# Kernel tuning notes

Hardware: AMD Instinct MI355X
Metric: run time of the kernel (lower is better)

## Reference

```python
import jax, jax.numpy as jnp
import numpy as np

D_MODEL = 1024
D_INNER = 2 * D_MODEL          # expand=2
D_STATE = 16
D_CONV = 4
DT_RANK = D_MODEL // 16        # ceil(1024/16)
BATCH, SEQ = 4, 1024
LN_EPS = 1e-5
LRELU_SLOPE = 0.01


def setup_inputs() -> dict:
    key = jax.random.key(0)
    ks = jax.random.split(key, 12)
    s = 0.02
    return {
        "x": jax.random.normal(ks[0], (BATCH, SEQ, D_MODEL), jnp.float32),
        "W_in": jax.random.normal(ks[1], (D_MODEL, 2 * D_INNER), jnp.float32) * s,
        "conv_w": jax.random.normal(ks[2], (D_INNER, D_CONV), jnp.float32) * s,
        "conv_b": jnp.zeros((D_INNER,), jnp.float32),
        "W_x": jax.random.normal(ks[3], (D_INNER, DT_RANK + 2 * D_STATE), jnp.float32) * s,
        "W_dt": jax.random.normal(ks[4], (DT_RANK, D_INNER), jnp.float32) * s,
        "b_dt": jax.random.normal(ks[5], (D_INNER,), jnp.float32) * 0.1 - 4.0,
        "A_log": jnp.log(jnp.broadcast_to(jnp.arange(1, D_STATE + 1, dtype=jnp.float32), (D_INNER, D_STATE))),
        "D": jnp.ones((D_INNER,), jnp.float32),
        "W_out": jax.random.normal(ks[6], (D_INNER, D_MODEL), jnp.float32) * s,
        "gamma": jnp.ones((D_MODEL,), jnp.float32),
        "beta": jnp.zeros((D_MODEL,), jnp.float32),
    }


def _selective_scan(u, dt, A, B, C, Dp):
    # u, dt: (b, l, d); A: (d, n); B, C: (b, l, n); Dp: (d,)
    dA = jnp.exp(dt[..., None] * A)                       # (b, l, d, n)
    dBu = dt[..., None] * B[:, :, None, :] * u[..., None]  # (b, l, d, n)

    def step(h, inp):
        dA_t, dBu_t, C_t = inp                            # (b,d,n),(b,d,n),(b,n)
        h = dA_t * h + dBu_t
        y = jnp.einsum("bdn,bn->bd", h, C_t)
        return h, y

    h0 = jnp.zeros((u.shape[0], u.shape[2], A.shape[1]), u.dtype)
    xs = (dA.transpose(1, 0, 2, 3), dBu.transpose(1, 0, 2, 3), C.transpose(1, 0, 2))
    _, ys = jax.lax.scan(step, h0, xs)                    # ys: (l, b, d)
    return ys.transpose(1, 0, 2) + u * Dp                 # (b, l, d)


def _mamba(x, W_in, conv_w, conv_b, W_x, W_dt, b_dt, A_log, Dp, W_out):
    xz = x @ W_in                                          # (b, l, 2*di)
    xc, z = jnp.split(xz, 2, axis=-1)
    # causal depthwise conv over time
    xc_t = xc.transpose(0, 2, 1)                           # (b, di, l)
    kern = conv_w[:, None, :]                              # (di, 1, k)
    conv = jax.lax.conv_general_dilated(
        xc_t, kern, window_strides=(1,), padding=[(D_CONV - 1, 0)],
        dimension_numbers=("NCH", "OIH", "NCH"), feature_group_count=D_INNER)
    xc = jax.nn.silu(conv + conv_b[None, :, None]).transpose(0, 2, 1)  # (b, l, di)

    x_dbl = xc @ W_x                                       # (b, l, dt_rank + 2n)
    dt, Bm, Cm = jnp.split(x_dbl, [DT_RANK, DT_RANK + D_STATE], axis=-1)
    dt = jax.nn.softplus(dt @ W_dt + b_dt)                 # (b, l, di)
    A = -jnp.exp(A_log)                                    # (di, n)

    y = _selective_scan(xc, dt, A, Bm, Cm, Dp)             # (b, l, di)
    y = y * jax.nn.silu(z)
    return y @ W_out                                       # (b, l, d_model)


def reference(x, W_in, conv_w, conv_b, W_x, W_dt, b_dt, A_log, D, W_out, gamma, beta):
    h = x + _mamba(x, W_in, conv_w, conv_b, W_x, W_dt, b_dt, A_log, D, W_out)
    mu = jnp.mean(h, axis=-1, keepdims=True)
    var = jnp.mean(jnp.square(h - mu), axis=-1, keepdims=True)
    h = (h - mu) * jax.lax.rsqrt(var + LN_EPS) * gamma + beta
    return jnp.where(h >= 0, h, LRELU_SLOPE * h)
```

## Files before the change

kernel.cpp:

```cpp
#include <hip/hip_runtime.h>
#include <hip/hip_fp16.h>
#include <cstdint>
#include <cstddef>

typedef _Float16 f16x8 __attribute__((ext_vector_type(8)));
typedef _Float16 f16x4 __attribute__((ext_vector_type(4)));
typedef float    f32x4 __attribute__((ext_vector_type(4)));

#define TC  32
#define NCH 32

__device__ __forceinline__ float sigmoidf_(float x) { return 1.f / (1.f + __expf(-x)); }

__device__ __forceinline__ void gload_lds16(const _Float16* g, _Float16* l) {
  __builtin_amdgcn_global_load_lds(
      (const __attribute__((address_space(1))) void*)g,
      (__attribute__((address_space(3))) void*)l, 16, 0, 0);
}

__device__ __forceinline__ void t16_body(const float* __restrict__ src,
    _Float16* __restrict__ dst, int R, int C, int Cpad, int bx, int by,
    int tid, float tile[32][33]) {
  int c0 = bx * 32, r0 = by * 32, tx = tid & 31, ty = tid >> 5;
  #pragma unroll
  for (int i = 0; i < 4; ++i) {
    int r = r0 + ty + i * 8, c = c0 + tx;
    tile[ty + i * 8][tx] = (r < R && c < C) ? src[(size_t)r * C + c] : 0.f;
  }
  __syncthreads();
  #pragma unroll
  for (int i = 0; i < 4; ++i) {
    int cc = c0 + ty + i * 8, rr = r0 + tx;
    if (cc < Cpad && rr < R) dst[(size_t)cc * R + rr] = (_Float16)tile[tx][ty + i * 8];
  }
}

__global__ __launch_bounds__(256) void k_prep(
    const float* __restrict__ x, _Float16* __restrict__ x16,
    const float* __restrict__ W_in, _Float16* __restrict__ WinT,
    const float* __restrict__ W_x, _Float16* __restrict__ WxT,
    const float* __restrict__ W_dt, _Float16* __restrict__ WdtT,
    const float* __restrict__ W_out, _Float16* __restrict__ WoutT)
{
  __shared__ float tile[32][33];
  const int blk = blockIdx.x, tid = threadIdx.x;
  if (blk < 4096) {
    int i = blk * 256 + tid;
    float4 v = ((const float4*)x)[i];
    f16x4 o = {(_Float16)v.x, (_Float16)v.y, (_Float16)v.z, (_Float16)v.w};
    ((f16x4*)x16)[i] = o;
  } else if (blk < 8192) {
    int b = blk - 4096;
    t16_body(W_in, WinT, 1024, 4096, 4096, b & 127, b >> 7, tid, tile);
  } else if (blk < 8448) {
    int b = blk - 8192;
    t16_body(W_x, WxT, 2048, 96, 128, b & 3, b >> 2, tid, tile);
  } else if (blk < 8576) {
    int b = blk - 8448;
    t16_body(W_dt, WdtT, 64, 2048, 2048, b & 63, b >> 6, tid, tile);
  } else {
    int b = blk - 8576;
    t16_body(W_out, WoutT, 2048, 1024, 1024, b & 31, b >> 5, tid, tile);
  }
}

template <int EPI>
__global__ __launch_bounds__(256) void k_gemm_bt(
    const _Float16* __restrict__ A,
    const _Float16* __restrict__ BT,
    float* __restrict__ C,
    _Float16* __restrict__ C16,
    _Float16* __restrict__ AUX,
    int M, int N, int K)
{
  __shared__ __align__(16) _Float16 As[128 * 64];
  __shared__ __align__(16) _Float16 Bs[128 * 64];
  const int tid  = threadIdx.x;
  const int lane = tid & 63;
  const int wave = tid >> 6;
  const int wm = (wave >> 1) * 64;
  const int wn = (wave & 1) * 64;
  const int l15 = lane & 15;
  const int q   = lane >> 4;
  const int m0 = blockIdx.y * 128;
  const int n0 = blockIdx.x * 128;

  const int kpb = K / gridDim.z;
  const int k0  = blockIdx.z * kpb;

  const int rch = lane >> 3;
  const int g   = (lane & 7) ^ (rch & 7);
  const _Float16* gA = A  + (size_t)(m0 + wave * 32 + rch) * K + k0 + g * 8;
  const _Float16* gB = BT + (size_t)(n0 + wave * 32 + rch) * K + k0 + g * 8;
  _Float16* lA = As + wave * 32 * 64 + lane * 8;
  _Float16* lB = Bs + wave * 32 * 64 + lane * 8;

  const int sx = l15 & 7;

  f32x4 acc[4][4] = {};

  for (int k = 0; k < kpb; k += 64) {
    #pragma unroll
    for (int c = 0; c < 4; ++c) {
      gload_lds16(gA + (size_t)(c * 8) * K + k, lA + c * 512);
      gload_lds16(gB + (size_t)(c * 8) * K + k, lB + c * 512);
    }
    __syncthreads();
    #pragma unroll
    for (int k32 = 0; k32 < 2; ++k32) {
      f16x8 af[4], bf[4];
      #pragma unroll
      for (int i = 0; i < 4; ++i) {
        af[i] = *(const f16x8*)&As[(wm + i * 16 + l15) * 64 + ((k32 * 4 + q) ^ sx) * 8];
        bf[i] = *(const f16x8*)&Bs[(wn + i * 16 + l15) * 64 + ((k32 * 4 + q) ^ sx) * 8];
      }
      #pragma unroll
      for (int mi = 0; mi < 4; ++mi)
        #pragma unroll
        for (int ni = 0; ni < 4; ++ni)
          acc[mi][ni] = __builtin_amdgcn_mfma_f32_16x16x32_f16(af[mi], bf[ni], acc[mi][ni], 0, 0, 0);
    }
    __syncthreads();
  }

  #pragma unroll
  for (int mi = 0; mi < 4; ++mi) {
    #pragma unroll
    for (int ni = 0; ni < 4; ++ni) {
      int col = n0 + wn + ni * 16 + l15;
      #pragma unroll
      for (int r = 0; r < 4; ++r) {
        int row = m0 + wm + mi * 16 + q * 4 + r;
        float v = acc[mi][ni][r];
        if constexpr (EPI == 3) {
          if (col < 2048) {
            C16[(size_t)row * 2048 + col] = (_Float16)v;
          } else {
            AUX[(size_t)row * 2048 + (col - 2048)] = (_Float16)(v * sigmoidf_(v));
          }
        } else {
          C[(size_t)blockIdx.z * M * N + (size_t)row * N + col] = v;
        }
      }
    }
  }
}

__global__ __launch_bounds__(256) void k_g3(
    const float* __restrict__ Cpart,
    const _Float16* __restrict__ BT,
    const float* __restrict__ bias,
    _Float16* __restrict__ AUX)
{
  __shared__ __align__(16) _Float16 As2[128 * 72];
  __shared__ __align__(16) _Float16 Bs[128 * 64];
  const int tid  = threadIdx.x;
  const int lane = tid & 63;
  const int wave = tid >> 6;
  const int wm = (wave >> 1) * 64;
  const int wn = (wave & 1) * 64;
  const int l15 = lane & 15;
  const int q   = lane >> 4;
  const int m0 = blockIdx.y * 128;
  const int n0 = blockIdx.x * 128;
  const int PL = 4096 * 128;

  #pragma unroll
  for (int i = 0; i < 4; ++i) {
    int idx = i * 256 + tid;
    int r = idx >> 3, s = idx & 7;
    const float* p = Cpart + (size_t)(m0 + r) * 128 + s * 8;
    f16x8 o;
    #pragma unroll
    for (int j = 0; j < 8; ++j)
      o[j] = (_Float16)(p[j] + p[j + PL] + p[j + 2 * PL] + p[j + 3 * PL]);
    *(f16x8*)&As2[r * 72 + s * 8] = o;
  }
  const int rch = lane >> 3;
  const int g   = (lane & 7) ^ (rch & 7);
  const _Float16* gB = BT + (size_t)(n0 + wave * 32 + rch) * 64 + g * 8;
  _Float16* lB = Bs + wave * 32 * 64 + lane * 8;
  #pragma unroll
  for (int c = 0; c < 4; ++c)
    gload_lds16(gB + (size_t)(c * 8) * 64, lB + c * 512);
  __syncthreads();

  const int sx = l15 & 7;
  f32x4 acc[4][4] = {};
  #pragma unroll
  for (int k32 = 0; k32 < 2; ++k32) {
    f16x8 af[4], bf[4];
    #pragma unroll
    for (int i = 0; i < 4; ++i) {
      af[i] = *(const f16x8*)&As2[(wm + i * 16 + l15) * 72 + (k32 * 4 + q) * 8];
      bf[i] = *(const f16x8*)&Bs[(wn + i * 16 + l15) * 64 + ((k32 * 4 + q) ^ sx) * 8];
    }
    #pragma unroll
    for (int mi = 0; mi < 4; ++mi)
      #pragma unroll
      for (int ni = 0; ni < 4; ++ni)
        acc[mi][ni] = __builtin_amdgcn_mfma_f32_16x16x32_f16(af[mi], bf[ni], acc[mi][ni], 0, 0, 0);
  }

  #pragma unroll
  for (int mi = 0; mi < 4; ++mi) {
    #pragma unroll
    for (int ni = 0; ni < 4; ++ni) {
      int col = n0 + wn + ni * 16 + l15;
      #pragma unroll
      for (int r = 0; r < 4; ++r) {
        int row = m0 + wm + mi * 16 + q * 4 + r;
        float t = acc[mi][ni][r] + bias[col];
        float sp = (t > 20.f) ? t : log1pf(__expf(t));
        AUX[(size_t)row * 2048 + col] = (_Float16)sp;
      }
    }
  }
}

__global__ __launch_bounds__(256) void k_conv_silu(
    const _Float16* __restrict__ xc, const float* __restrict__ cw,
    const float* __restrict__ cb, _Float16* __restrict__ out)
{
  int idx = blockIdx.x * 256 + threadIdx.x;
  int d = idx & 2047;
  int row = idx >> 11;
  int t = row & 1023;
  const _Float16* p = xc + (size_t)row * 2048 + d;
  float acc = cb[d] + cw[d * 4 + 3] * (float)p[0];
  if (t >= 1) acc += cw[d * 4 + 2] * (float)p[-2048];
  if (t >= 2) acc += cw[d * 4 + 1] * (float)p[-4096];
  if (t >= 3) acc += cw[d * 4 + 0] * (float)p[-6144];
  out[idx] = (_Float16)(acc * sigmoidf_(acc));
}

__global__ __launch_bounds__(256) void k_scan_part(
    const _Float16* __restrict__ dt, const _Float16* __restrict__ u,
    const float* __restrict__ Cpart, const float* __restrict__ A_log,
    float* __restrict__ P, float* __restrict__ S)
{
  const int tid = threadIdx.x;
  const int d = blockIdx.x * 256 + tid;
  const int c = blockIdx.y;
  const int b = blockIdx.z;
  const int row0 = b * 1024 + c * TC;
  const int PL = 4096 * 128;
  __shared__ float Bs[TC * 16];
  for (int i = tid; i < TC * 16; i += 256) {
    int t = i >> 4, n = i & 15;
    const float* p = Cpart + (size_t)(row0 + t) * 128 + 64 + n;
    Bs[i] = p[0] + p[PL] + p[2 * PL] + p[3 * PL];
  }
  float a[16];
  #pragma unroll
  for (int n = 0; n < 16; ++n) a[n] = -__expf(A_log[d * 16 + n]);
  float h[16] = {};
  float sumdt = 0.f;
  __syncthreads();
  for (int t = 0; t < TC; ++t) {
    const int row = row0 + t;
    float dtv = (float)dt[(size_t)row * 2048 + d];
    float uv  = (float)u[(size_t)row * 2048 + d];
    float dtu = dtv * uv;
    sumdt += dtv;
    #pragma unroll
    for (int n = 0; n < 16; ++n)
      h[n] = h[n] * __expf(dtv * a[n]) + dtu * Bs[t * 16 + n];
  }
  const size_t base = (size_t)(b * NCH + c) * 16 * 2048 + d;
  #pragma unroll
  for (int n = 0; n < 16; ++n) {
    P[base + n * 2048] = __expf(sumdt * a[n]);
    S[base + n * 2048] = h[n];
  }
}

__global__ __launch_bounds__(256) void k_scan_comb(
    float* __restrict__ P, const float* __restrict__ S)
{
  int idx = blockIdx.x * 256 + threadIdx.x;
  int d = idx & 2047;
  int n = (idx >> 11) & 15;
  int b = idx >> 15;
  float H = 0.f;
  for (int c = 0; c < NCH - 1; ++c) {
    size_t off = ((size_t)(b * NCH + c) * 16 + n) * 2048 + d;
    H = P[off] * H + S[off];
    P[off] = H;
  }
}

__global__ __launch_bounds__(256) void k_scan_y(
    const _Float16* dt, const _Float16* __restrict__ u,
    const _Float16* __restrict__ zs, const float* __restrict__ Cpart,
    const float* __restrict__ A_log, const float* __restrict__ Hbuf,
    const float* __restrict__ Dv, _Float16* ys)
{
  const int tid = threadIdx.x;
  const int d = blockIdx.x * 256 + tid;
  const int c = blockIdx.y;
  const int b = blockIdx.z;
  const int row0 = b * 1024 + c * TC;
  const int PL = 4096 * 128;
  __shared__ float Bs[TC * 16], Cs[TC * 16];
  for (int i = tid; i < TC * 16; i += 256) {
    int t = i >> 4, n = i & 15;
    const float* p = Cpart + (size_t)(row0 + t) * 128 + 64 + n;
    Bs[i] = p[0] + p[PL] + p[2 * PL] + p[3 * PL];
    Cs[i] = p[16] + p[16 + PL] + p[16 + 2 * PL] + p[16 + 3 * PL];
  }
  float a[16];
  #pragma unroll
  for (int n = 0; n < 16; ++n) a[n] = -__expf(A_log[d * 16 + n]);
  float h[16];
  if (c == 0) {
    #pragma unroll
    for (int n = 0; n < 16; ++n) h[n] = 0.f;
  } else {
    const size_t hb = (size_t)(b * NCH + (c - 1)) * 16 * 2048 + d;
    #pragma unroll
    for (int n = 0; n < 16; ++n) h[n] = Hbuf[hb + n * 2048];
  }
  const float Dd = Dv[d];
  __syncthreads();
  for (int t = 0; t < TC; ++t) {
    const int row = row0 + t;
    float dtv = (float)dt[(size_t)row * 2048 + d];
    float uv  = (float)u[(size_t)row * 2048 + d];
    float zv  = (float)zs[(size_t)row * 2048 + d];
    float dtu = dtv * uv;
    float y = uv * Dd;
    #pragma unroll
    for (int n = 0; n < 16; ++n) {
      h[n] = h[n] * __expf(dtv * a[n]) + dtu * Bs[t * 16 + n];
      y = fmaf(h[n], Cs[t * 16 + n], y);
    }
    ys[(size_t)row * 2048 + d] = (_Float16)(y * zv);
  }
}

__global__ __launch_bounds__(256) void k_resid_ln(
    const float* __restrict__ x, const float* __restrict__ yp,
    const float* __restrict__ gamma, const float* __restrict__ beta,
    float* __restrict__ out)
{
  int row = blockIdx.x;
  int tid = threadIdx.x;
  const int PL = 4096 * 1024;
  float v[4];
  float s = 0.f, s2 = 0.f;
  #pragma unroll
  for (int i = 0; i < 4; ++i) {
    int c = tid + i * 256;
    size_t off = (size_t)row * 1024 + c;
    float h = x[off] + yp[off] + yp[off + PL];
    v[i] = h; s += h; s2 += h * h;
  }
  #pragma unroll
  for (int off = 32; off > 0; off >>= 1) {
    s  += __shfl_down(s, off, 64);
    s2 += __shfl_down(s2, off, 64);
  }
  __shared__ float rs[4], rs2[4];
  int wv = tid >> 6, ln = tid & 63;
  if (ln == 0) { rs[wv] = s; rs2[wv] = s2; }
  __syncthreads();
  if (tid == 0) {
    float a = 0.f, b2 = 0.f;
    #pragma unroll
    for (int i = 0; i < 4; ++i) { a += rs[i]; b2 += rs2[i]; }
    rs[0] = a; rs2[0] = b2;
  }
  __syncthreads();
  float mu  = rs[0] * (1.f / 1024.f);
  float var = rs2[0] * (1.f / 1024.f) - mu * mu;
  float inv = rsqrtf(var + 1e-5f);
  #pragma unroll
  for (int i = 0; i < 4; ++i) {
    int c = tid + i * 256;
    float hn = (v[i] - mu) * inv * gamma[c] + beta[c];
    out[(size_t)row * 1024 + c] = hn >= 0.f ? hn : 0.01f * hn;
  }
}

extern "C" void kernel_launch(void* const* d_in, const int* in_sizes, int n_in,
                              void* d_out, int out_size, void* d_ws, size_t ws_size,
                              hipStream_t stream)
{
  const float* x     = (const float*)d_in[0];
  const float* W_in  = (const float*)d_in[1];
  const float* convw = (const float*)d_in[2];
  const float* convb = (const float*)d_in[3];
  const float* W_x   = (const float*)d_in[4];
  const float* W_dt  = (const float*)d_in[5];
  const float* b_dt  = (const float*)d_in[6];
  const float* A_log = (const float*)d_in[7];
  const float* Dv    = (const float*)d_in[8];
  const float* W_out = (const float*)d_in[9];
  const float* gamma = (const float*)d_in[10];
  const float* beta  = (const float*)d_in[11];
  float* out = (float*)d_out;

  char* ws = (char*)d_ws;
  const size_t MB = 1ull << 20;
  _Float16* x16   = (_Float16*)(ws + 0 * MB);
  _Float16* WinT  = (_Float16*)(ws + 8 * MB);
  _Float16* xc16  = (_Float16*)(ws + 16 * MB);
  _Float16* zsil  = (_Float16*)(ws + 32 * MB);
  _Float16* xcs   = (_Float16*)(ws + 48 * MB);
  _Float16* dtb   = (_Float16*)(ws + 64 * MB);
  _Float16* WxT   = (_Float16*)(ws + 80 * MB);
  _Float16* WdtT  = (_Float16*)(ws + 80 * MB + 512 * 1024);
  _Float16* WoutT = (_Float16*)(ws + 81 * MB);
  float*    Cpart = (float*)   (ws + 85 * MB);
  float*    Pb    = (float*)   (ws + 0 * MB);
  float*    Sb    = (float*)   (ws + 16 * MB);
  _Float16* ysb   = dtb;
  float*    yp    = (float*)   (ws + 0 * MB);

  k_prep<<<10624, 256, 0, stream>>>(x, x16, W_in, WinT, W_x, WxT, W_dt, WdtT, W_out, WoutT);
  k_gemm_bt<3><<<dim3(32, 32), 256, 0, stream>>>(x16, WinT, nullptr, xc16, zsil, 4096, 4096, 1024);
  k_conv_silu<<<4096 * 2048 / 256, 256, 0, stream>>>(xc16, convw, convb, xcs);
  k_gemm_bt<4><<<dim3(1, 32, 4), 256, 0, stream>>>(xcs, WxT, Cpart, nullptr, nullptr, 4096, 128, 2048);
  k_g3<<<dim3(16, 32), 256, 0, stream>>>(Cpart, WdtT, b_dt, dtb);
  k_scan_part<<<dim3(8, NCH, 4), 256, 0, stream>>>(dtb, xcs, Cpart, A_log, Pb, Sb);
  k_scan_comb<<<4 * 16 * 2048 / 256, 256, 0, stream>>>(Pb, Sb);
  k_scan_y<<<dim3(8, NCH, 4), 256, 0, stream>>>(dtb, xcs, zsil, Cpart, A_log, Pb, Dv, ysb);
  k_gemm_bt<4><<<dim3(8, 32, 2), 256, 0, stream>>>(ysb, WoutT, yp, nullptr, nullptr, 4096, 1024, 2048);
  k_resid_ln<<<4096, 256, 0, stream>>>(x, yp, gamma, beta, out);
}
```

Baseline: 375.5 us.

## Vectorize conv and LayerNorm, pre-reduce split-K partials, retune scan chunks and out-proj split

This bundles several separate changes. The causal conv now loads eight channels per thread using pre-transposed fp16 weights. A new reduction kernel collapses the four split-K partials of the x_proj GEMM once, so the generic GEMM (with a new softplus epilogue) can replace the custom dt-projection kernel and the scan kernels stop re-summing partials. The scan chunk length doubles to 64 while the number of chunks halves. The output projection moves to 4-way split-K, and the residual LayerNorm is vectorized with float4. The out-proj split adds extra partial-buffer traffic in exchange for more parallelism, and the longer chunks lengthen each sequential scan segment.

Measured after the change: 372.5 us. No clear change (-0.8%).

```diff
diff --git a/kernel.cpp b/kernel.cpp
--- a/kernel.cpp
+++ b/kernel.cpp
@@ -7,8 +7,8 @@
 typedef _Float16 f16x4 __attribute__((ext_vector_type(4)));
 typedef float    f32x4 __attribute__((ext_vector_type(4)));
 
-#define TC  32
-#define NCH 32
+#define TC  64
+#define NCH 16
 
 __device__ __forceinline__ float sigmoidf_(float x) { return 1.f / (1.f + __expf(-x)); }
 
@@ -40,7 +40,8 @@
     const float* __restrict__ W_in, _Float16* __restrict__ WinT,
     const float* __restrict__ W_x, _Float16* __restrict__ WxT,
     const float* __restrict__ W_dt, _Float16* __restrict__ WdtT,
-    const float* __restrict__ W_out, _Float16* __restrict__ WoutT)
+    const float* __restrict__ W_out, _Float16* __restrict__ WoutT,
+    const float* __restrict__ convw, _Float16* __restrict__ cwT)
 {
   __shared__ float tile[32][33];
   const int blk = blockIdx.x, tid = threadIdx.x;
@@ -58,9 +59,16 @@
   } else if (blk < 8576) {
     int b = blk - 8448;
     t16_body(W_dt, WdtT, 64, 2048, 2048, b & 63, b >> 6, tid, tile);
-  } else {
+  } else if (blk < 10624) {
     int b = blk - 8576;
     t16_body(W_out, WoutT, 2048, 1024, 1024, b & 31, b >> 5, tid, tile);
+  } else {
+    #pragma unroll
+    for (int j = 0; j < 32; ++j) {
+      int idx = j * 256 + tid;
+      int tap = idx >> 11, d = idx & 2047;
+      cwT[idx] = (_Float16)convw[d * 4 + tap];
+    }
   }
 }
 
@@ -71,6 +79,7 @@
     float* __restrict__ C,
     _Float16* __restrict__ C16,
     _Float16* __restrict__ AUX,
+    const float* __restrict__ bias,
     int M, int N, int K)
 {
   __shared__ __align__(16) _Float16 As[128 * 64];
@@ -132,7 +141,11 @@
       for (int r = 0; r < 4; ++r) {
         int row = m0 + wm + mi * 16 + q * 4 + r;
         float v = acc[mi][ni][r];
-        if constexpr (EPI == 3) {
+        if constexpr (EPI == 2) {
+          float t = v + bias[col];
+          float sp = (t > 20.f) ? t : log1pf(__expf(t));
+          AUX[(size_t)row * N + col] = (_Float16)sp;
+        } else if constexpr (EPI == 3) {
           if (col < 2048) {
             C16[(size_t)row * 2048 + col] = (_Float16)v;
           } else {
@@ -146,97 +159,59 @@
   }
 }
 
-__global__ __launch_bounds__(256) void k_g3(
-    const float* __restrict__ Cpart,
-    const _Float16* __restrict__ BT,
-    const float* __restrict__ bias,
-    _Float16* __restrict__ AUX)
-{
-  __shared__ __align__(16) _Float16 As2[128 * 72];
-  __shared__ __align__(16) _Float16 Bs[128 * 64];
-  const int tid  = threadIdx.x;
-  const int lane = tid & 63;
-  const int wave = tid >> 6;
-  const int wm = (wave >> 1) * 64;
-  const int wn = (wave & 1) * 64;
-  const int l15 = lane & 15;
-  const int q   = lane >> 4;
-  const int m0 = blockIdx.y * 128;
-  const int n0 = blockIdx.x * 128;
+__global__ __launch_bounds__(256) void k_red(const float* __restrict__ Cp,
+                                             _Float16* __restrict__ dtin,
+                                             float* __restrict__ xbc) {
+  int i = blockIdx.x * 256 + threadIdx.x;
   const int PL = 4096 * 128;
-
-  #pragma unroll
-  for (int i = 0; i < 4; ++i) {
-    int idx = i * 256 + tid;
-    int r = idx >> 3, s = idx & 7;
-    const float* p = Cpart + (size_t)(m0 + r) * 128 + s * 8;
-    f16x8 o;
-    #pragma unroll
-    for (int j = 0; j < 8; ++j)
-      o[j] = (_Float16)(p[j] + p[j + PL] + p[j + 2 * PL] + p[j + 3 * PL]);
-    *(f16x8*)&As2[r * 72 + s * 8] = o;
-  }
-  const int rch = lane >> 3;
-  const int g   = (lane & 7) ^ (rch & 7);
-  const _Float16* gB = BT + (size_t)(n0 + wave * 32 + rch) * 64 + g * 8;
-  _Float16* lB = Bs + wave * 32 * 64 + lane * 8;
-  #pragma unroll
-  for (int c = 0; c < 4; ++c)
-    gload_lds16(gB + (size_t)(c * 8) * 64, lB + c * 512);
-  __syncthreads();
-
-  const int sx = l15 & 7;
-  f32x4 acc[4][4] = {};
-  #pragma unroll
-  for (int k32 = 0; k32 < 2; ++k32) {
-    f16x8 af[4], bf[4];
-    #pragma unroll
-    for (int i = 0; i < 4; ++i) {
-      af[i] = *(const f16x8*)&As2[(wm + i * 16 + l15) * 72 + (k32 * 4 + q) * 8];
-      bf[i] = *(const f16x8*)&Bs[(wn + i * 16 + l15) * 64 + ((k32 * 4 + q) ^ sx) * 8];
-    }
-    #pragma unroll
-    for (int mi = 0; mi < 4; ++mi)
-      #pragma unroll
-      for (int ni = 0; ni < 4; ++ni)
-        acc[mi][ni] = __builtin_amdgcn_mfma_f32_16x16x32_f16(af[mi], bf[ni], acc[mi][ni], 0, 0, 0);
-  }
-
-  #pragma unroll
-  for (int mi = 0; mi < 4; ++mi) {
-    #pragma unroll
-    for (int ni = 0; ni < 4; ++ni) {
-      int col = n0 + wn + ni * 16 + l15;
-      #pragma unroll
-      for (int r = 0; r < 4; ++r) {
-        int row = m0 + wm + mi * 16 + q * 4 + r;
-        float t = acc[mi][ni][r] + bias[col];
-        float sp = (t > 20.f) ? t : log1pf(__expf(t));
-        AUX[(size_t)row * 2048 + col] = (_Float16)sp;
-      }
-    }
-  }
+  float s = Cp[i] + Cp[i + PL] + Cp[i + 2 * PL] + Cp[i + 3 * PL];
+  int col = i & 127, row = i >> 7;
+  if (col < 64) dtin[(size_t)row * 64 + col] = (_Float16)s;
+  else if (col < 96) xbc[(size_t)row * 32 + (col - 64)] = s;
 }
 
 __global__ __launch_bounds__(256) void k_conv_silu(
-    const _Float16* __restrict__ xc, const float* __restrict__ cw,
+    const _Float16* __restrict__ xc, const _Float16* __restrict__ cwT,
     const float* __restrict__ cb, _Float16* __restrict__ out)
 {
-  int idx = blockIdx.x * 256 + threadIdx.x;
-  int d = idx & 2047;
-  int row = idx >> 11;
-  int t = row & 1023;
-  const _Float16* p = xc + (size_t)row * 2048 + d;
-  float acc = cb[d] + cw[d * 4 + 3] * (float)p[0];
-  if (t >= 1) acc += cw[d * 4 + 2] * (float)p[-2048];
-  if (t >= 2) acc += cw[d * 4 + 1] * (float)p[-4096];
-  if (t >= 3) acc += cw[d * 4 + 0] * (float)p[-6144];
-  out[idx] = (_Float16)(acc * sigmoidf_(acc));
+  const int row = blockIdx.x;
+  const int t = row & 1023;
+  const int d8 = threadIdx.x;
+  const size_t base = (size_t)row * 2048 + d8 * 8;
+  f16x8 p0 = *(const f16x8*)&xc[base];
+  f16x8 w3 = *(const f16x8*)&cwT[3 * 2048 + d8 * 8];
+  float4 cb0 = ((const float4*)cb)[d8 * 2];
+  float4 cb1 = ((const float4*)cb)[d8 * 2 + 1];
+  float accv[8] = {cb0.x, cb0.y, cb0.z, cb0.w, cb1.x, cb1.y, cb1.z, cb1.w};
+  #pragma unroll
+  for (int j = 0; j < 8; ++j) accv[j] += (float)w3[j] * (float)p0[j];
+  if (t >= 1) {
+    f16x8 p = *(const f16x8*)&xc[base - 2048];
+    f16x8 w = *(const f16x8*)&cwT[2 * 2048 + d8 * 8];
+    #pragma unroll
+    for (int j = 0; j < 8; ++j) accv[j] += (float)w[j] * (float)p[j];
+  }
+  if (t >= 2) {
+    f16x8 p = *(const f16x8*)&xc[base - 4096];
+    f16x8 w = *(const f16x8*)&cwT[1 * 2048 + d8 * 8];
+    #pragma unroll
+    for (int j = 0; j < 8; ++j) accv[j] += (float)w[j] * (float)p[j];
+  }
+  if (t >= 3) {
+    f16x8 p = *(const f16x8*)&xc[base - 6144];
+    f16x8 w = *(const f16x8*)&cwT[0 * 2048 + d8 * 8];
+    #pragma unroll
+    for (int j = 0; j < 8; ++j) accv[j] += (float)w[j] * (float)p[j];
+  }
+  f16x8 o;
+  #pragma unroll
+  for (int j = 0; j < 8; ++j) o[j] = (_Float16)(accv[j] * sigmoidf_(accv[j]));
+  *(f16x8*)&out[base] = o;
 }
 
 __global__ __launch_bounds__(256) void k_scan_part(
     const _Float16* __restrict__ dt, const _Float16* __restrict__ u,
-    const float* __restrict__ Cpart, const float* __restrict__ A_log,
+    const float* __restrict__ xbc, const float* __restrict__ A_log,
     float* __restrict__ P, float* __restrict__ S)
 {
   const int tid = threadIdx.x;
@@ -244,12 +219,10 @@
   const int c = blockIdx.y;
   const int b = blockIdx.z;
   const int row0 = b * 1024 + c * TC;
-  const int PL = 4096 * 128;
   __shared__ float Bs[TC * 16];
   for (int i = tid; i < TC * 16; i += 256) {
     int t = i >> 4, n = i & 15;
-    const float* p = Cpart + (size_t)(row0 + t) * 128 + 64 + n;
-    Bs[i] = p[0] + p[PL] + p[2 * PL] + p[3 * PL];
+    Bs[i] = xbc[(size_t)(row0 + t) * 32 + n];
   }
   float a[16];
   #pragma unroll
@@ -292,7 +265,7 @@
 
 __global__ __launch_bounds__(256) void k_scan_y(
     const _Float16* dt, const _Float16* __restrict__ u,
-    const _Float16* __restrict__ zs, const float* __restrict__ Cpart,
+    const _Float16* __restrict__ zs, const float* __restrict__ xbc,
     const float* __restrict__ A_log, const float* __restrict__ Hbuf,
     const float* __restrict__ Dv, _Float16* ys)
 {
@@ -301,13 +274,11 @@
   const int c = blockIdx.y;
   const int b = blockIdx.z;
   const int row0 = b * 1024 + c * TC;
-  const int PL = 4096 * 128;
   __shared__ float Bs[TC * 16], Cs[TC * 16];
   for (int i = tid; i < TC * 16; i += 256) {
     int t = i >> 4, n = i & 15;
-    const float* p = Cpart + (size_t)(row0 + t) * 128 + 64 + n;
-    Bs[i] = p[0] + p[PL] + p[2 * PL] + p[3 * PL];
-    Cs[i] = p[16] + p[16 + PL] + p[16 + 2 * PL] + p[16 + 3 * PL];
+    Bs[i] = xbc[(size_t)(row0 + t) * 32 + n];
+    Cs[i] = xbc[(size_t)(row0 + t) * 32 + 16 + n];
   }
   float a[16];
   #pragma unroll
@@ -346,16 +317,19 @@
 {
   int row = blockIdx.x;
   int tid = threadIdx.x;
-  const int PL = 4096 * 1024;
-  float v[4];
-  float s = 0.f, s2 = 0.f;
-  #pragma unroll
-  for (int i = 0; i < 4; ++i) {
-    int c = tid + i * 256;
-    size_t off = (size_t)row * 1024 + c;
-    float h = x[off] + yp[off] + yp[off + PL];
-    v[i] = h; s += h; s2 += h * h;
-  }
+  const int PL4 = 4096 * 256;
+  const int o4 = row * 256 + tid;
+  float4 xv = ((const float4*)x)[o4];
+  float4 p0 = ((const float4*)yp)[o4];
+  float4 p1 = ((const float4*)yp)[o4 + PL4];
+  float4 p2 = ((const float4*)yp)[o4 + 2 * PL4];
+  float4 p3 = ((const float4*)yp)[o4 + 3 * PL4];
+  float v[4] = {xv.x + p0.x + p1.x + p2.x + p3.x,
+                xv.y + p0.y + p1.y + p2.y + p3.y,
+                xv.z + p0.z + p1.z + p2.z + p3.z,
+                xv.w + p0.w + p1.w + p2.w + p3.w};
+  float s = v[0] + v[1] + v[2] + v[3];
+  float s2 = v[0]*v[0] + v[1]*v[1] + v[2]*v[2] + v[3]*v[3];
   #pragma unroll
   for (int off = 32; off > 0; off >>= 1) {
     s  += __shfl_down(s, off, 64);
@@ -375,12 +349,18 @@
   float mu  = rs[0] * (1.f / 1024.f);
   float var = rs2[0] * (1.f / 1024.f) - mu * mu;
   float inv = rsqrtf(var + 1e-5f);
+  float4 gv = ((const float4*)gamma)[tid];
+  float4 bv = ((const float4*)beta)[tid];
+  float gg[4] = {gv.x, gv.y, gv.z, gv.w};
+  float bb[4] = {bv.x, bv.y, bv.z, bv.w};
+  float4 ov;
+  float* op = (float*)&ov;
   #pragma unroll
   for (int i = 0; i < 4; ++i) {
-    int c = tid + i * 256;
-    float hn = (v[i] - mu) * inv * gamma[c] + beta[c];
-    out[(size_t)row * 1024 + c] = hn >= 0.f ? hn : 0.01f * hn;
-  }
+    float hn = (v[i] - mu) * inv * gg[i] + bb[i];
+    op[i] = hn >= 0.f ? hn : 0.01f * hn;
+  }
+  ((float4*)out)[o4] = ov;
 }
 
 extern "C" void kernel_launch(void* const* d_in, const int* in_sizes, int n_in,
@@ -413,19 +393,24 @@
   _Float16* WdtT  = (_Float16*)(ws + 80 * MB + 512 * 1024);
   _Float16* WoutT = (_Float16*)(ws + 81 * MB);
   float*    Cpart = (float*)   (ws + 85 * MB);
+  float*    xbc   = (float*)   (ws + 93 * MB);
+  _Float16* dtin  = (_Float16*)(ws + 93 * MB + 512 * 1024);
+  _Float16* cwT   = (_Float16*)(ws + 94 * MB);
   float*    Pb    = (float*)   (ws + 0 * MB);
-  float*    Sb    = (float*)   (ws + 16 * MB);
+  float*    Sb    = (float*)   (ws + 8 * MB);
   _Float16* ysb   = dtb;
   float*    yp    = (float*)   (ws + 0 * MB);
 
-  k_prep<<<10624, 256, 0, stream>>>(x, x16, W_in, WinT, W_x, WxT, W_dt, WdtT, W_out, WoutT);
-  k_gemm_bt<3><<<dim3(32, 32), 256, 0, stream>>>(x16, WinT, nullptr, xc16, zsil, 4096, 4096, 1024);
-  k_conv_silu<<<4096 * 2048 / 256, 256, 0, stream>>>(xc16, convw, convb, xcs);
-  k_gemm_bt<4><<<dim3(1, 32, 4), 256, 0, stream>>>(xcs, WxT, Cpart, nullptr, nullptr, 4096, 128, 2048);
-  k_g3<<<dim3(16, 32), 256, 0, stream>>>(Cpart, WdtT, b_dt, dtb);
-  k_scan_part<<<dim3(8, NCH, 4), 256, 0, stream>>>(dtb, xcs, Cpart, A_log, Pb, Sb);
+  k_prep<<<10625, 256, 0, stream>>>(x, x16, W_in, WinT, W_x, WxT, W_dt, WdtT,
+                                    W_out, WoutT, convw, cwT);
+  k_gemm_bt<3><<<dim3(32, 32), 256, 0, stream>>>(x16, WinT, nullptr, xc16, zsil, nullptr, 4096, 4096, 1024);
+  k_conv_silu<<<4096, 256, 0, stream>>>(xc16, cwT, convb, xcs);
+  k_gemm_bt<4><<<dim3(1, 32, 4), 256, 0, stream>>>(xcs, WxT, Cpart, nullptr, nullptr, nullptr, 4096, 128, 2048);
+  k_red<<<4096 * 128 / 256, 256, 0, stream>>>(Cpart, dtin, xbc);
+  k_gemm_bt<2><<<dim3(16, 32), 256, 0, stream>>>(dtin, WdtT, nullptr, nullptr, dtb, b_dt, 4096, 2048, 64);
+  k_scan_part<<<dim3(8, NCH, 4), 256, 0, stream>>>(dtb, xcs, xbc, A_log, Pb, Sb);
   k_scan_comb<<<4 * 16 * 2048 / 256, 256, 0, stream>>>(Pb, Sb);
-  k_scan_y<<<dim3(8, NCH, 4), 256, 0, stream>>>(dtb, xcs, zsil, Cpart, A_log, Pb, Dv, ysb);
-  k_gemm_bt<4><<<dim3(8, 32, 2), 256, 0, stream>>>(ysb, WoutT, yp, nullptr, nullptr, 4096, 1024, 2048);
+  k_scan_y<<<dim3(8, NCH, 4), 256, 0, stream>>>(dtb, xcs, zsil, xbc, A_log, Pb, Dv, ysb);
+  k_gemm_bt<4><<<dim3(8, 32, 4), 256, 0, stream>>>(ysb, WoutT, yp, nullptr, nullptr, nullptr, 4096, 1024, 2048);
   k_resid_ln<<<4096, 256, 0, stream>>>(x, yp, gamma, beta, out);
 }
```
